# Kernel optimization log

Measured on AMD Instinct MI355X. Metric: run time of the kernel, lower is better.

The kernel has to match this reference:

```python
import jax, jax.numpy as jnp
import numpy as np

N = 100000   # nodes
E = 6400000  # edges (avg degree 64)
IN, H, OUT, C = 2, 16, 8, 1000


def _gcn_conv(x, src, dst, dinv, W, b):
    # PyG GCNConv: out = D^{-1/2} (A+I) D^{-1/2} X W + b, messages flow src->dst.
    h = x @ W                              # [N, F_out]
    norm = dinv[src] * dinv[dst]           # [E]
    agg = jax.ops.segment_sum(h[src] * norm[:, None], dst, num_segments=N)
    agg = agg + h * (dinv * dinv)[:, None]  # self-loop contribution
    return agg + b


def setup_inputs() -> dict:
    key = jax.random.key(0)
    ks = jax.random.split(key, 9)
    s = 1.0 / np.sqrt(H)
    return {
        "x": jax.random.normal(ks[0], (N, IN), jnp.float32),
        "edge_index": jax.random.randint(ks[1], (2, E), 0, N, jnp.int32),
        "W1": jax.random.normal(ks[2], (IN, H), jnp.float32) * (1.0 / np.sqrt(IN)),
        "b1": jnp.zeros((H,), jnp.float32),
        "W2": jax.random.normal(ks[3], (H, OUT), jnp.float32) * s,
        "b2": jnp.zeros((OUT,), jnp.float32),
        "Wfc": jax.random.normal(ks[4], (OUT, C), jnp.float32) * (1.0 / np.sqrt(OUT)),
        "bfc": jnp.zeros((C,), jnp.float32),
    }


def reference(x, edge_index, W1, b1, W2, b2, Wfc, bfc):
    src, dst = edge_index[0], edge_index[1]
    # degree with self-loops added (deg >= 1, so no inf masking needed)
    deg = jax.ops.segment_sum(jnp.ones((E,), jnp.float32), dst, num_segments=N) + 1.0
    dinv = jax.lax.rsqrt(deg)
    h = jax.nn.relu(_gcn_conv(x, src, dst, dinv, W1, b1))
    h = _gcn_conv(h, src, dst, dinv, W2, b2)
    return h @ Wfc + bfc  # [N, C]
```

## Files before the change

### kernel.cpp

```cpp
#include <hip/hip_runtime.h>


#define RSH 7
#define RNB 128
#define NBMAX 1024
#define CAPB 8960
#define CHB 16384

__global__ void k_init(int* __restrict__ gcur, int B) {
    int t = blockIdx.x * blockDim.x + threadIdx.x;
    if (t < B) gcur[t] = t * CAPB;
}

__global__ void __launch_bounds__(512) k_bin(const int* __restrict__ src, const int* __restrict__ dst,
                                             int* __restrict__ gcur, int* __restrict__ binned,
                                             int E, int B) {
    __shared__ int hist[NBMAX];
    __shared__ int base[NBMAX];
    int tid = threadIdx.x;
    int e0 = blockIdx.x * CHB;
    int n = E - e0; if (n > CHB) n = CHB;
    for (int t = tid; t < B; t += 512) hist[t] = 0;
    __syncthreads();
    for (int k = tid; k < n; k += 512) atomicAdd(&hist[dst[e0 + k] >> RSH], 1);
    __syncthreads();
    for (int t = tid; t < B; t += 512) {
        int h = hist[t];
        base[t] = h ? atomicAdd(&gcur[t], h) : 0;
        hist[t] = 0;
    }
    __syncthreads();
    for (int k = tid; k < n; k += 512) {
        int d = dst[e0 + k], s = src[e0 + k];
        int b = d >> RSH;
        int pos = base[b] + atomicAdd(&hist[b], 1);
        if (pos < (b + 1) * CAPB)
            binned[pos] = ((d & (RNB - 1)) << 17) | s;
    }
}

__global__ void __launch_bounds__(256) k_degsort(const int* __restrict__ gcur, int* __restrict__ binned,
                                                 const float* __restrict__ x, float* __restrict__ dinv,
                                                 float* __restrict__ xs, int* __restrict__ offS,
                                                 int* __restrict__ offE, int N) {
    __shared__ int buf[CAPB];
    __shared__ int deg[RNB];
    __shared__ int cur[RNB];
    __shared__ int wtot[2];
    int tid = threadIdx.x, b = blockIdx.x;
    int beg = b * CAPB;
    int end = gcur[b]; int cap = beg + CAPB; if (end > cap) end = cap;
    int cnt = end - beg;
    if (tid < RNB) deg[tid] = 0;
    __syncthreads();
    for (int k = tid; k < cnt; k += 256) {
        int p = binned[beg + k];
        buf[k] = p;
        atomicAdd(&deg[p >> 17], 1);
    }
    __syncthreads();
    int lane = tid & 63;
    int v = 0, incl = 0;
    if (tid < RNB) {
        v = deg[tid];
        incl = v;
#pragma unroll
        for (int d = 1; d < 64; d <<= 1) {
            int t = __shfl_up(incl, d);
            if (lane >= d) incl += t;
        }
        if (lane == 63) wtot[tid >> 6] = incl;
    }
    __syncthreads();
    if (tid < RNB) {
        int excl = ((tid >= 64) ? wtot[0] : 0) + incl - v;
        cur[tid] = beg + excl;
        int i = b * RNB + tid;
        if (i < N) {
            offS[i] = beg + excl;
            offE[i] = beg + excl + v;
            float dv = rsqrtf((float)v + 1.0f);
            dinv[i] = dv;
            float2 xv = *reinterpret_cast<const float2*>(x + 2 * (size_t)i);
            float2 o; o.x = xv.x * dv; o.y = xv.y * dv;
            *reinterpret_cast<float2*>(xs + 2 * (size_t)i) = o;
        }
    }
    __syncthreads();
    for (int k = tid; k < cnt; k += 256) {
        int p = buf[k];
        int pos = atomicAdd(&cur[p >> 17], 1);
        binned[pos] = p & 0x1FFFF;
    }
}

__global__ void k_l1(const int* __restrict__ offS, const int* __restrict__ offE,
                     const int* __restrict__ csr, const float* __restrict__ xs,
                     const float* __restrict__ x, const float* __restrict__ dinv,
                     const float* __restrict__ W1, const float* __restrict__ b1,
                     const float* __restrict__ W2,
                     float* __restrict__ h2lin, float* __restrict__ h2s, int N) {
    int gid = blockIdx.x * blockDim.x + threadIdx.x;
    int i = gid >> 6, lane = gid & 63;
    if (i >= N) return;
    int beg = offS[i], end = offE[i];
    float a0 = 0.f, a1 = 0.f;
    for (int e = beg + lane; e < end; e += 64) {
        int s = csr[e];
        float2 v = *reinterpret_cast<const float2*>(xs + 2 * (size_t)s);
        a0 += v.x; a1 += v.y;
    }
#pragma unroll
    for (int d = 32; d > 0; d >>= 1) { a0 += __shfl_xor(a0, d); a1 += __shfl_xor(a1, d); }
    if (lane == 0) {
        float dv = dinv[i], dv2 = dv * dv;
        float z0 = dv * a0 + x[2 * (size_t)i] * dv2;
        float z1 = dv * a1 + x[2 * (size_t)i + 1] * dv2;
        float acc[8];
#pragma unroll
        for (int g = 0; g < 8; ++g) acc[g] = 0.f;
#pragma unroll
        for (int f = 0; f < 16; ++f) {
            float h = fmaf(z0, W1[f], fmaf(z1, W1[16 + f], b1[f]));
            h = fmaxf(h, 0.f);
#pragma unroll
            for (int g = 0; g < 8; ++g) acc[g] = fmaf(h, W2[f * 8 + g], acc[g]);
        }
        float4* o = reinterpret_cast<float4*>(h2lin + 8 * (size_t)i);
        o[0] = make_float4(acc[0], acc[1], acc[2], acc[3]);
        o[1] = make_float4(acc[4], acc[5], acc[6], acc[7]);
        float4* o2 = reinterpret_cast<float4*>(h2s + 8 * (size_t)i);
        o2[0] = make_float4(acc[0] * dv, acc[1] * dv, acc[2] * dv, acc[3] * dv);
        o2[1] = make_float4(acc[4] * dv, acc[5] * dv, acc[6] * dv, acc[7] * dv);
    }
}

__global__ void k_l2(const int* __restrict__ offS, const int* __restrict__ offE,
                     const int* __restrict__ csr, const float* __restrict__ h2s,
                     const float* __restrict__ h2lin, const float* __restrict__ dinv,
                     const float* __restrict__ b2, float* __restrict__ zfin, int N) {
    int gid = blockIdx.x * blockDim.x + threadIdx.x;
    int i = gid >> 6, lane = gid & 63;
    if (i >= N) return;
    int beg = offS[i], end = offE[i];
    float a[8];
#pragma unroll
    for (int g = 0; g < 8; ++g) a[g] = 0.f;
    for (int e = beg + lane; e < end; e += 64) {
        int s = csr[e];
        const float4* p = reinterpret_cast<const float4*>(h2s + 8 * (size_t)s);
        float4 u = p[0], w = p[1];
        a[0] += u.x; a[1] += u.y; a[2] += u.z; a[3] += u.w;
        a[4] += w.x; a[5] += w.y; a[6] += w.z; a[7] += w.w;
    }
#pragma unroll
    for (int g = 0; g < 8; ++g) {
#pragma unroll
        for (int d = 32; d > 0; d >>= 1) a[g] += __shfl_xor(a[g], d);
    }
    if (lane == 0) {
        float dv = dinv[i], dv2 = dv * dv;
        const float4* hl = reinterpret_cast<const float4*>(h2lin + 8 * (size_t)i);
        float4 h0 = hl[0], h1v = hl[1];
        float4 r0, r1;
        r0.x = dv * a[0] + h0.x * dv2 + b2[0];
        r0.y = dv * a[1] + h0.y * dv2 + b2[1];
        r0.z = dv * a[2] + h0.z * dv2 + b2[2];
        r0.w = dv * a[3] + h0.w * dv2 + b2[3];
        r1.x = dv * a[4] + h1v.x * dv2 + b2[4];
        r1.y = dv * a[5] + h1v.y * dv2 + b2[5];
        r1.z = dv * a[6] + h1v.z * dv2 + b2[6];
        r1.w = dv * a[7] + h1v.w * dv2 + b2[7];
        float4* o = reinterpret_cast<float4*>(zfin + 8 * (size_t)i);
        o[0] = r0; o[1] = r1;
    }
}

__global__ void k_final(const float* __restrict__ zfin, const float* __restrict__ Wfc,
                        const float* __restrict__ bfc, float* __restrict__ out, int N, int C) {
    __shared__ float sh[64];
    int i0 = blockIdx.x * 8;
    int t = threadIdx.x;
    if (t < 64) {
        int i = i0 + (t >> 3);
        sh[t] = (i < N) ? zfin[8 * (size_t)i + (t & 7)] : 0.f;
    }
    __syncthreads();
    int c4 = t * 4;
    if (c4 + 4 <= C) {
        float4 w[8];
#pragma unroll
        for (int f = 0; f < 8; ++f)
            w[f] = *reinterpret_cast<const float4*>(Wfc + (size_t)f * C + c4);
        float4 bias = *reinterpret_cast<const float4*>(bfc + c4);
#pragma unroll 1
        for (int k = 0; k < 8; ++k) {
            int i = i0 + k;
            if (i >= N) break;
            float4 acc = bias;
#pragma unroll
            for (int f = 0; f < 8; ++f) {
                float hv = sh[k * 8 + f];
                acc.x = fmaf(hv, w[f].x, acc.x);
                acc.y = fmaf(hv, w[f].y, acc.y);
                acc.z = fmaf(hv, w[f].z, acc.z);
                acc.w = fmaf(hv, w[f].w, acc.w);
            }
            *reinterpret_cast<float4*>(out + (size_t)i * C + c4) = acc;
        }
    }
}

extern "C" void kernel_launch(void* const* d_in, const int* in_sizes, int n_in,
                              void* d_out, int out_size, void* d_ws, size_t ws_size,
                              hipStream_t stream) {
    const float* x   = (const float*)d_in[0];
    const int*   ei  = (const int*)d_in[1];
    const float* W1  = (const float*)d_in[2];
    const float* b1  = (const float*)d_in[3];
    const float* W2  = (const float*)d_in[4];
    const float* b2  = (const float*)d_in[5];
    const float* Wfc = (const float*)d_in[6];
    const float* bfc = (const float*)d_in[7];
    float* out = (float*)d_out;

    const int N = in_sizes[0] / 2;
    const int E = in_sizes[1] / 2;
    const int C = in_sizes[7];
    const int* src = ei;
    const int* dst = ei + E;

    const int B = (N + RNB - 1) >> RSH;

    size_t NP = (size_t)((N + 16) & ~15);
    int* gcur   = (int*)d_ws;
    int* binned = gcur + NBMAX;
    int* offS   = binned + (size_t)B * CAPB;
    int* offE   = offS + NP;
    float* fb    = (float*)(offE + NP);
    float* dinv  = fb;
    float* xs    = dinv + NP;
    float* h2lin = xs + 2 * NP;
    float* h2s   = h2lin + 8 * NP;
    float* zfin  = h2s + 8 * NP;

    k_init<<<(B + 255) / 256, 256, 0, stream>>>(gcur, B);
    k_bin<<<(E + CHB - 1) / CHB, 512, 0, stream>>>(src, dst, gcur, binned, E, B);
    k_degsort<<<B, 256, 0, stream>>>(gcur, binned, x, dinv, xs, offS, offE, N);
    {
        long long tot = (long long)N * 64;
        k_l1<<<(int)((tot + 255) / 256), 256, 0, stream>>>(offS, offE, binned, xs, x, dinv,
                                                           W1, b1, W2, h2lin, h2s, N);
        k_l2<<<(int)((tot + 255) / 256), 256, 0, stream>>>(offS, offE, binned, h2s, h2lin,
                                                           dinv, b2, zfin, N);
    }
    k_final<<<(N + 7) / 8, 256, 0, stream>>>(zfin, Wfc, bfc, out, N, C);
}
```

Before: 717.2 us.

## Fuse layer-2 aggregation into final linear kernel and sort bins in LDS

The layer-2 neighbour aggregation is merged into the final dense projection kernel. Each 256-thread block aggregates 8 nodes (two per wavefront) into shared memory, then computes the 1000-wide output, which removes the zfin round-trip and one launch. In the degree-sort kernel, the scatter now targets shared memory and is written back to global coalesced, replacing scattered global stores with a re-read of binned input and an extra sync. The fused kernel has 4 waves per block doing sequential aggregation, which may reduce latency hiding compared with the previous one-wave-per-node launch.

```diff
diff --git a/kernel.cpp b/kernel.cpp
--- a/kernel.cpp
+++ b/kernel.cpp
@@ -53,11 +53,8 @@
     int cnt = end - beg;
     if (tid < RNB) deg[tid] = 0;
     __syncthreads();
-    for (int k = tid; k < cnt; k += 256) {
-        int p = binned[beg + k];
-        buf[k] = p;
-        atomicAdd(&deg[p >> 17], 1);
-    }
+    for (int k = tid; k < cnt; k += 256)
+        atomicAdd(&deg[binned[beg + k] >> 17], 1);
     __syncthreads();
     int lane = tid & 63;
     int v = 0, incl = 0;
@@ -74,7 +71,7 @@
     __syncthreads();
     if (tid < RNB) {
         int excl = ((tid >= 64) ? wtot[0] : 0) + incl - v;
-        cur[tid] = beg + excl;
+        cur[tid] = excl;
         int i = b * RNB + tid;
         if (i < N) {
             offS[i] = beg + excl;
@@ -88,10 +85,13 @@
     }
     __syncthreads();
     for (int k = tid; k < cnt; k += 256) {
-        int p = buf[k];
+        int p = binned[beg + k];
         int pos = atomicAdd(&cur[p >> 17], 1);
-        binned[pos] = p & 0x1FFFF;
-    }
+        buf[pos] = p & 0x1FFFF;
+    }
+    __syncthreads();
+    for (int k = tid; k < cnt; k += 256)
+        binned[beg + k] = buf[k];
 }
 
 __global__ void k_l1(const int* __restrict__ offS, const int* __restrict__ offE,
@@ -135,58 +135,53 @@
     }
 }
 
-__global__ void k_l2(const int* __restrict__ offS, const int* __restrict__ offE,
-                     const int* __restrict__ csr, const float* __restrict__ h2s,
-                     const float* __restrict__ h2lin, const float* __restrict__ dinv,
-                     const float* __restrict__ b2, float* __restrict__ zfin, int N) {
-    int gid = blockIdx.x * blockDim.x + threadIdx.x;
-    int i = gid >> 6, lane = gid & 63;
-    if (i >= N) return;
-    int beg = offS[i], end = offE[i];
-    float a[8];
-#pragma unroll
-    for (int g = 0; g < 8; ++g) a[g] = 0.f;
-    for (int e = beg + lane; e < end; e += 64) {
-        int s = csr[e];
-        const float4* p = reinterpret_cast<const float4*>(h2s + 8 * (size_t)s);
-        float4 u = p[0], w = p[1];
-        a[0] += u.x; a[1] += u.y; a[2] += u.z; a[3] += u.w;
-        a[4] += w.x; a[5] += w.y; a[6] += w.z; a[7] += w.w;
-    }
-#pragma unroll
-    for (int g = 0; g < 8; ++g) {
-#pragma unroll
-        for (int d = 32; d > 0; d >>= 1) a[g] += __shfl_xor(a[g], d);
-    }
-    if (lane == 0) {
-        float dv = dinv[i], dv2 = dv * dv;
-        const float4* hl = reinterpret_cast<const float4*>(h2lin + 8 * (size_t)i);
-        float4 h0 = hl[0], h1v = hl[1];
-        float4 r0, r1;
-        r0.x = dv * a[0] + h0.x * dv2 + b2[0];
-        r0.y = dv * a[1] + h0.y * dv2 + b2[1];
-        r0.z = dv * a[2] + h0.z * dv2 + b2[2];
-        r0.w = dv * a[3] + h0.w * dv2 + b2[3];
-        r1.x = dv * a[4] + h1v.x * dv2 + b2[4];
-        r1.y = dv * a[5] + h1v.y * dv2 + b2[5];
-        r1.z = dv * a[6] + h1v.z * dv2 + b2[6];
-        r1.w = dv * a[7] + h1v.w * dv2 + b2[7];
-        float4* o = reinterpret_cast<float4*>(zfin + 8 * (size_t)i);
-        o[0] = r0; o[1] = r1;
-    }
-}
-
-__global__ void k_final(const float* __restrict__ zfin, const float* __restrict__ Wfc,
-                        const float* __restrict__ bfc, float* __restrict__ out, int N, int C) {
+__global__ void __launch_bounds__(256) k_l2f(const int* __restrict__ offS, const int* __restrict__ offE,
+                                             const int* __restrict__ csr, const float* __restrict__ h2s,
+                                             const float* __restrict__ h2lin, const float* __restrict__ dinv,
+                                             const float* __restrict__ b2, const float* __restrict__ Wfc,
+                                             const float* __restrict__ bfc, float* __restrict__ out,
+                                             int N, int C) {
     __shared__ float sh[64];
     int i0 = blockIdx.x * 8;
-    int t = threadIdx.x;
-    if (t < 64) {
-        int i = i0 + (t >> 3);
-        sh[t] = (i < N) ? zfin[8 * (size_t)i + (t & 7)] : 0.f;
-    }
-    __syncthreads();
-    int c4 = t * 4;
+    int tid = threadIdx.x, wid = tid >> 6, lane = tid & 63;
+#pragma unroll
+    for (int u = 0; u < 2; ++u) {
+        int k = 2 * wid + u;
+        int i = i0 + k;
+        if (i < N) {
+            int beg = offS[i], end = offE[i];
+            float a[8];
+#pragma unroll
+            for (int g = 0; g < 8; ++g) a[g] = 0.f;
+            for (int e = beg + lane; e < end; e += 64) {
+                int s = csr[e];
+                const float4* p = reinterpret_cast<const float4*>(h2s + 8 * (size_t)s);
+                float4 u4 = p[0], w4 = p[1];
+                a[0] += u4.x; a[1] += u4.y; a[2] += u4.z; a[3] += u4.w;
+                a[4] += w4.x; a[5] += w4.y; a[6] += w4.z; a[7] += w4.w;
+            }
+#pragma unroll
+            for (int g = 0; g < 8; ++g) {
+#pragma unroll
+                for (int d = 32; d > 0; d >>= 1) a[g] += __shfl_xor(a[g], d);
+            }
+            if (lane == 0) {
+                float dv = dinv[i], dv2 = dv * dv;
+                const float4* hl = reinterpret_cast<const float4*>(h2lin + 8 * (size_t)i);
+                float4 h0 = hl[0], h1v = hl[1];
+                sh[k * 8 + 0] = dv * a[0] + h0.x * dv2 + b2[0];
+                sh[k * 8 + 1] = dv * a[1] + h0.y * dv2 + b2[1];
+                sh[k * 8 + 2] = dv * a[2] + h0.z * dv2 + b2[2];
+                sh[k * 8 + 3] = dv * a[3] + h0.w * dv2 + b2[3];
+                sh[k * 8 + 4] = dv * a[4] + h1v.x * dv2 + b2[4];
+                sh[k * 8 + 5] = dv * a[5] + h1v.y * dv2 + b2[5];
+                sh[k * 8 + 6] = dv * a[6] + h1v.z * dv2 + b2[6];
+                sh[k * 8 + 7] = dv * a[7] + h1v.w * dv2 + b2[7];
+            }
+        }
+    }
+    __syncthreads();
+    int c4 = tid * 4;
     if (c4 + 4 <= C) {
         float4 w[8];
 #pragma unroll
@@ -242,7 +237,6 @@
     float* xs    = dinv + NP;
     float* h2lin = xs + 2 * NP;
     float* h2s   = h2lin + 8 * NP;
-    float* zfin  = h2s + 8 * NP;
 
     k_init<<<(B + 255) / 256, 256, 0, stream>>>(gcur, B);
     k_bin<<<(E + CHB - 1) / CHB, 512, 0, stream>>>(src, dst, gcur, binned, E, B);
@@ -251,8 +245,7 @@
         long long tot = (long long)N * 64;
         k_l1<<<(int)((tot + 255) / 256), 256, 0, stream>>>(offS, offE, binned, xs, x, dinv,
                                                            W1, b1, W2, h2lin, h2s, N);
-        k_l2<<<(int)((tot + 255) / 256), 256, 0, stream>>>(offS, offE, binned, h2s, h2lin,
-                                                           dinv, b2, zfin, N);
-    }
-    k_final<<<(N + 7) / 8, 256, 0, stream>>>(zfin, Wfc, bfc, out, N, C);
-}
+    }
+    k_l2f<<<(N + 7) / 8, 256, 0, stream>>>(offS, offE, binned, h2s, h2lin, dinv, b2,
+                                           Wfc, bfc, out, N, C);
+}
```

Result: faster. 691.1 us (-3.6%).
